# Performance work log

Measured on AMD Instinct MI355X. Metric: run time of the kernel, lower is better.

The kernel has to match this reference:

```python
import jax, jax.numpy as jnp
import numpy as np

N_NODES = 50000
N_EDGES = 800000
H = 128   # atom_hidden_feats
B = 64    # bond_in_feats
NEG_SLOPE = 0.01  # torch LeakyReLU default


def setup_inputs() -> dict:
    key = jax.random.key(0)
    k1, k2, k3, k4, k5 = jax.random.split(key, 5)
    feat = jax.random.normal(k1, (N_NODES, H), dtype=jnp.float32)
    gdf_feat = jax.random.normal(k2, (N_EDGES, B), dtype=jnp.float32)
    # Linear(2H+B -> H): weight [H, 2H+B], bias [H]
    W = jax.random.normal(k3, (H, 2 * H + B), dtype=jnp.float32) * 0.05
    b = jnp.zeros((H,), dtype=jnp.float32)
    src = jax.random.randint(k4, (N_EDGES,), 0, N_NODES, dtype=jnp.int64)
    dst = jax.random.randint(k5, (N_EDGES,), 0, N_NODES, dtype=jnp.int64)
    return {"feat": feat, "gdf_feat": gdf_feat, "W": W, "b": b, "src": src, "dst": dst}


def reference(feat, gdf_feat, W, b, src, dst):
    n_nodes = feat.shape[0]
    # Per-edge message: concat(src_feat, dst_feat, edge_feat) -> linear -> gate
    z = jnp.concatenate([feat[src], feat[dst], gdf_feat], axis=-1)  # [E, 2H+B]
    z = z @ W.T + b                                                 # [E, H]
    msg = jax.nn.sigmoid(z) * jnp.where(z > 0, z, NEG_SLOPE * z)    # sigmoid * leaky_relu
    # Scatter-sum messages to destination nodes
    return jax.ops.segment_sum(msg, dst, num_segments=n_nodes)      # [N, H]
```

## Files before the change

### kernel.cpp

```cpp
#include <hip/hip_runtime.h>
#include <hip/hip_bf16.h>

typedef __attribute__((ext_vector_type(8)))  short bf16x8;
typedef __attribute__((ext_vector_type(16))) float f32x16;
typedef __attribute__((ext_vector_type(4)))  float f32x4;
typedef __attribute__((ext_vector_type(2)))  __fp16 fp16x2;

#define NN 50000
#define EE 800000
#define HH 128
#define KK 320
#define NEG 0.01f
#define NTILES (EE / 64)
#define NBLK 512
#define ACC_BYTES ((size_t)NN * HH * 2)

__device__ __forceinline__ unsigned pack2(float a, float b) {
    unsigned short lo = __builtin_bit_cast(unsigned short, __float2bfloat16(a));
    unsigned short hi = __builtin_bit_cast(unsigned short, __float2bfloat16(b));
    return (unsigned)lo | ((unsigned)hi << 16);
}

__global__ __launch_bounds__(256) void featcvt_kernel(const float* __restrict__ feat,
                                                      ushort* __restrict__ featb)
{
    const int t = blockIdx.x * 256 + threadIdx.x;
    const float* p = feat + (long long)t * 8;
    f32x4 v0 = *(const f32x4*)p;
    f32x4 v1 = *(const f32x4*)(p + 4);
    int4 h;
    h.x = (int)pack2(v0[0], v0[1]); h.y = (int)pack2(v0[2], v0[3]);
    h.z = (int)pack2(v1[0], v1[1]); h.w = (int)pack2(v1[2], v1[3]);
    *(int4*)(featb + (long long)t * 8) = h;
}

__global__ __launch_bounds__(256, 2) void fused_pipe_kernel(
    const ushort* __restrict__ featb, const float* __restrict__ gdf,
    const float*  __restrict__ W,     const float* __restrict__ bias,
    const int*    __restrict__ src,   const int*   __restrict__ dst,
    __fp16* __restrict__ acc16)
{
    __shared__ int4 lds4[2][64 * 40];
    __shared__ int  dsts[2][64];

    const int tid  = threadIdx.x;
    const int lane = tid & 63;
    const int wid  = tid >> 6;
    const int col  = wid * 32 + (lane & 31);
    const int khalf = lane >> 5;
    const int r = tid >> 2, q = tid & 3;

    bf16x8 Wb[20];
    {
        const float* wrow = W + col * KK + khalf * 8;
        #pragma unroll
        for (int k = 0; k < 20; k++) {
            f32x4 x0 = *(const f32x4*)(wrow + k * 16);
            f32x4 x1 = *(const f32x4*)(wrow + k * 16 + 4);
            union { bf16x8 v; unsigned u[4]; } t;
            t.u[0] = pack2(x0[0], x0[1]); t.u[1] = pack2(x0[2], x0[3]);
            t.u[2] = pack2(x1[0], x1[1]); t.u[3] = pack2(x1[2], x1[3]);
            Wb[k] = t.v;
        }
    }
    const float bv = bias[col];

    int4  sf[8];
    f32x4 sg[4];
    int   dStage;

    auto issueLoads = [&](int t, int s_i, int d_i) {
        const ushort* fs = featb + (long long)s_i * HH;
        const ushort* fd = featb + (long long)d_i * HH;
        const float*  ge = gdf + ((long long)t * 64 + r) * 64;
        #pragma unroll
        for (int i = 0; i < 8; i++) {
            const int c = q + i * 4;
            sf[i] = *(const int4*)((c < 16) ? (fs + c * 8) : (fd + (c - 16) * 8));
        }
        #pragma unroll
        for (int i = 0; i < 2; i++) {
            const int cg = q + i * 4;
            sg[2 * i]     = *(const f32x4*)(ge + cg * 8);
            sg[2 * i + 1] = *(const f32x4*)(ge + cg * 8 + 4);
        }
    };
    auto writeStage = [&](int buf) {
        char* base = (char*)lds4[buf];
        const int xr = (r & 7) << 4;
        #pragma unroll
        for (int i = 0; i < 8; i++) {
            const int c = q + i * 4;
            *(int4*)(base + r * 640 + ((c * 16) ^ xr)) = sf[i];
        }
        #pragma unroll
        for (int i = 0; i < 2; i++) {
            const int c = 32 + q + i * 4;
            int4 h;
            h.x = (int)pack2(sg[2*i][0], sg[2*i][1]);
            h.y = (int)pack2(sg[2*i][2], sg[2*i][3]);
            h.z = (int)pack2(sg[2*i+1][0], sg[2*i+1][1]);
            h.w = (int)pack2(sg[2*i+1][2], sg[2*i+1][3]);
            *(int4*)(base + r * 640 + ((c * 16) ^ xr)) = h;
        }
        if (q == 0) dsts[buf][r] = dStage;
    };

    int tile = blockIdx.x;
    int sN = src[(long long)tile * 64 + r];
    int dN = dst[(long long)tile * 64 + r];
    issueLoads(tile, sN, dN);
    dStage = dN;
    int nt = tile + NBLK;
    {
        const int tc = (nt < NTILES) ? nt : 0;
        sN = src[(long long)tc * 64 + r];
        dN = dst[(long long)tc * 64 + r];
    }
    writeStage(0);
    __syncthreads();

    int cur = 0;
    const int arow = lane & 31;
    const int xa   = (arow & 7) << 4;

    while (true) {
        const bool hasNext = (nt < NTILES);
        if (hasNext) {
            issueLoads(nt, sN, dN);
            dStage = dN;
            const int nnt = nt + NBLK;
            const int tc = (nnt < NTILES) ? nnt : 0;
            sN = src[(long long)tc * 64 + r];
            dN = dst[(long long)tc * 64 + r];
        }

        char* abase = (char*)lds4[cur];
        f32x16 acc0 = {}; f32x16 acc1 = {};
        #pragma unroll
        for (int k = 0; k < 20; k++) {
            const int kb = k * 32 + khalf * 16;
            bf16x8 a0 = *(const bf16x8*)(abase + arow * 640 + (kb ^ xa));
            bf16x8 a1 = *(const bf16x8*)(abase + (arow + 32) * 640 + (kb ^ xa));
            acc0 = __builtin_amdgcn_mfma_f32_32x32x16_bf16(a0, Wb[k], acc0, 0, 0, 0);
            acc1 = __builtin_amdgcn_mfma_f32_32x32x16_bf16(a1, Wb[k], acc1, 0, 0, 0);
        }

        #pragma unroll
        for (int rt = 0; rt < 2; rt++) {
            const f32x16 A = rt ? acc1 : acc0;
            #pragma unroll
            for (int g = 0; g < 4; g++) {
                #pragma unroll
                for (int j = 0; j < 4; j++) {
                    const int reg = g * 4 + j;
                    const int row = j + g * 8 + khalf * 4;
                    const float z  = A[reg] + bv;
                    const float lr = z > 0.f ? z : NEG * z;
                    const float sg2 = 1.f / (1.f + __expf(-z));
                    const float m  = lr * sg2;
                    const float o  = __shfl_xor(m, 1);
                    const int dn = dsts[cur][rt * 32 + row];
                    if (!(lane & 1)) {
                        fp16x2 hv = __builtin_amdgcn_cvt_pkrtz(m, o);
                        __fp16* p = acc16 + (long long)dn * HH + col;
                        asm volatile("global_atomic_pk_add_f16 %0, %1, off"
                                     :: "v"(p), "v"(hv) : "memory");
                    }
                }
            }
        }

        if (!hasNext) break;
        writeStage(cur ^ 1);
        tile = nt; nt += NBLK; cur ^= 1;
        __syncthreads();
    }
}

__global__ __launch_bounds__(256) void fused_fallback_kernel(
    const float* __restrict__ feat, const float* __restrict__ gdf,
    const float* __restrict__ W,    const float* __restrict__ bias,
    const int*   __restrict__ src,  const int*   __restrict__ dst,
    float* __restrict__ out)
{
    __shared__ int4 lds4[64 * 40];
    __shared__ int  dsts[64];
    char* lds = (char*)lds4;
    const int tid = threadIdx.x, lane = tid & 63, wid = tid >> 6;
    const int col = wid * 32 + (lane & 31), khalf = lane >> 5;
    const int r = tid >> 2, q = tid & 3;
    const long long ebase = (long long)blockIdx.x * 64;

    bf16x8 Wb[20];
    {
        const float* wrow = W + col * KK + khalf * 8;
        #pragma unroll
        for (int k = 0; k < 20; k++) {
            f32x4 x0 = *(const f32x4*)(wrow + k * 16);
            f32x4 x1 = *(const f32x4*)(wrow + k * 16 + 4);
            union { bf16x8 v; unsigned u[4]; } t;
            t.u[0] = pack2(x0[0], x0[1]); t.u[1] = pack2(x0[2], x0[3]);
            t.u[2] = pack2(x1[0], x1[1]); t.u[3] = pack2(x1[2], x1[3]);
            Wb[k] = t.v;
        }
    }
    const int s = src[ebase + r], d = dst[ebase + r];
    if (q == 0) dsts[r] = d;
    {
        const float* fs = feat + (long long)s * HH;
        const float* fd = feat + (long long)d * HH;
        const float* ge = gdf + (ebase + r) * 64;
        #pragma unroll
        for (int i = 0; i < 10; i++) {
            const int c = q + i * 4;
            const float* p = (c < 16) ? (fs + c * 8)
                           : (c < 32) ? (fd + (c - 16) * 8)
                                      : (ge + (c - 32) * 8);
            f32x4 v0 = *(const f32x4*)p;
            f32x4 v1 = *(const f32x4*)(p + 4);
            int4 h;
            h.x = (int)pack2(v0[0], v0[1]); h.y = (int)pack2(v0[2], v0[3]);
            h.z = (int)pack2(v1[0], v1[1]); h.w = (int)pack2(v1[2], v1[3]);
            *(int4*)(lds + r * 640 + ((c * 16) ^ ((r & 7) << 4))) = h;
        }
    }
    __syncthreads();
    f32x16 acc0 = {}; f32x16 acc1 = {};
    const int arow = lane & 31, xa = (arow & 7) << 4;
    #pragma unroll
    for (int k = 0; k < 20; k++) {
        const int kb = k * 32 + khalf * 16;
        bf16x8 a0 = *(const bf16x8*)(lds + arow * 640 + (kb ^ xa));
        bf16x8 a1 = *(const bf16x8*)(lds + (arow + 32) * 640 + (kb ^ xa));
        acc0 = __builtin_amdgcn_mfma_f32_32x32x16_bf16(a0, Wb[k], acc0, 0, 0, 0);
        acc1 = __builtin_amdgcn_mfma_f32_32x32x16_bf16(a1, Wb[k], acc1, 0, 0, 0);
    }
    const float bv = bias[col];
    #pragma unroll
    for (int rt = 0; rt < 2; rt++) {
        const f32x16 A = rt ? acc1 : acc0;
        #pragma unroll
        for (int g = 0; g < 4; g++) {
            #pragma unroll
            for (int j = 0; j < 4; j++) {
                const int reg = g * 4 + j;
                const int row = j + g * 8 + khalf * 4;
                const float z  = A[reg] + bv;
                const float lr = z > 0.f ? z : NEG * z;
                const float sgm = 1.f / (1.f + __expf(-z));
                unsafeAtomicAdd(out + (long long)dsts[rt * 32 + row] * HH + col, lr * sgm);
            }
        }
    }
}

__global__ __launch_bounds__(256) void conv_kernel(const int4* __restrict__ acc,
                                                   float4* __restrict__ out)
{
    const int i = blockIdx.x * 256 + threadIdx.x;
    union { int4 v; __fp16 h[8]; } u;
    u.v = acc[i];
    float4 a, b;
    a.x = (float)u.h[0]; a.y = (float)u.h[1]; a.z = (float)u.h[2]; a.w = (float)u.h[3];
    b.x = (float)u.h[4]; b.y = (float)u.h[5]; b.z = (float)u.h[6]; b.w = (float)u.h[7];
    out[2 * i]     = a;
    out[2 * i + 1] = b;
}

extern "C" void kernel_launch(void* const* d_in, const int* in_sizes, int n_in,
                              void* d_out, int out_size, void* d_ws, size_t ws_size,
                              hipStream_t stream) {
    const float* feat = (const float*)d_in[0];
    const float* gdf  = (const float*)d_in[1];
    const float* W    = (const float*)d_in[2];
    const float* bias = (const float*)d_in[3];
    const int*   src  = (const int*)d_in[4];
    const int*   dst  = (const int*)d_in[5];
    float* out = (float*)d_out;

    __fp16* acc16 = (__fp16*)d_ws;
    ushort* featb = (ushort*)((char*)d_ws + ACC_BYTES);

    if (ws_size >= 2 * ACC_BYTES) {
        (void)hipMemsetAsync(d_ws, 0, ACC_BYTES, stream);
        featcvt_kernel<<<NN * HH / 8 / 256, 256, 0, stream>>>(feat, featb);
        fused_pipe_kernel<<<NBLK, 256, 0, stream>>>(featb, gdf, W, bias,
                                                    src, dst, acc16);
        conv_kernel<<<NN * HH / 8 / 256, 256, 0, stream>>>((const int4*)d_ws,
                                                           (float4*)out);
    } else {
        (void)hipMemsetAsync(out, 0, (size_t)out_size * sizeof(float), stream);
        fused_fallback_kernel<<<EE / 64, 256, 0, stream>>>(feat, gdf, W, bias,
                                                           src, dst, out);
    }
}
```

Before: 355.4 us.

## Single-buffer LDS stage to fit three blocks per CU with explicit barriers

Replaces the double-buffered LDS tile with a single buffer and guards it with explicit s_barrier plus lgkmcnt waits, which lets launch bounds rise to 3 blocks per CU and the persistent grid grow to 768 blocks. It also loads the four destination indices as one int4 and swaps the inline-asm packed fp16 atomic for unsafeAtomicAdd on __half2 with round-to-nearest conversion. The aim is more latency hiding for the gathers and atomics. In exchange it adds an extra barrier per tile, and the register cap that comes with 3 waves/SIMD may cause spills of the 20 W fragments.

```diff
diff --git a/kernel.cpp b/kernel.cpp
--- a/kernel.cpp
+++ b/kernel.cpp
@@ -1,10 +1,10 @@
 #include <hip/hip_runtime.h>
 #include <hip/hip_bf16.h>
+#include <hip/hip_fp16.h>
 
 typedef __attribute__((ext_vector_type(8)))  short bf16x8;
 typedef __attribute__((ext_vector_type(16))) float f32x16;
 typedef __attribute__((ext_vector_type(4)))  float f32x4;
-typedef __attribute__((ext_vector_type(2)))  __fp16 fp16x2;
 
 #define NN 50000
 #define EE 800000
@@ -12,7 +12,7 @@
 #define KK 320
 #define NEG 0.01f
 #define NTILES (EE / 64)
-#define NBLK 512
+#define NBLK 768
 #define ACC_BYTES ((size_t)NN * HH * 2)
 
 __device__ __forceinline__ unsigned pack2(float a, float b) {
@@ -34,14 +34,14 @@
     *(int4*)(featb + (long long)t * 8) = h;
 }
 
-__global__ __launch_bounds__(256, 2) void fused_pipe_kernel(
+__global__ __launch_bounds__(256, 3) void fused_pipe_kernel(
     const ushort* __restrict__ featb, const float* __restrict__ gdf,
     const float*  __restrict__ W,     const float* __restrict__ bias,
     const int*    __restrict__ src,   const int*   __restrict__ dst,
     __fp16* __restrict__ acc16)
 {
-    __shared__ int4 lds4[2][64 * 40];
-    __shared__ int  dsts[2][64];
+    __shared__ char lds[64 * 640 + 256];
+    int* dsts = (int*)(lds + 64 * 640);
 
     const int tid  = threadIdx.x;
     const int lane = tid & 63;
@@ -66,13 +66,13 @@
     const float bv = bias[col];
 
     int4  sf[8];
-    f32x4 sg[4];
+    f32x4 sgv[4];
     int   dStage;
 
-    auto issueLoads = [&](int t, int s_i, int d_i) {
+    auto issueLoads = [&](long long t, int s_i, int d_i) {
         const ushort* fs = featb + (long long)s_i * HH;
         const ushort* fd = featb + (long long)d_i * HH;
-        const float*  ge = gdf + ((long long)t * 64 + r) * 64;
+        const float*  ge = gdf + (t * 64 + r) * 64;
         #pragma unroll
         for (int i = 0; i < 8; i++) {
             const int c = q + i * 4;
@@ -81,46 +81,48 @@
         #pragma unroll
         for (int i = 0; i < 2; i++) {
             const int cg = q + i * 4;
-            sg[2 * i]     = *(const f32x4*)(ge + cg * 8);
-            sg[2 * i + 1] = *(const f32x4*)(ge + cg * 8 + 4);
+            sgv[2 * i]     = *(const f32x4*)(ge + cg * 8);
+            sgv[2 * i + 1] = *(const f32x4*)(ge + cg * 8 + 4);
         }
     };
-    auto writeStage = [&](int buf) {
-        char* base = (char*)lds4[buf];
+    auto writeStage = [&]() {
         const int xr = (r & 7) << 4;
         #pragma unroll
         for (int i = 0; i < 8; i++) {
             const int c = q + i * 4;
-            *(int4*)(base + r * 640 + ((c * 16) ^ xr)) = sf[i];
+            *(int4*)(lds + r * 640 + ((c * 16) ^ xr)) = sf[i];
         }
         #pragma unroll
         for (int i = 0; i < 2; i++) {
             const int c = 32 + q + i * 4;
             int4 h;
-            h.x = (int)pack2(sg[2*i][0], sg[2*i][1]);
-            h.y = (int)pack2(sg[2*i][2], sg[2*i][3]);
-            h.z = (int)pack2(sg[2*i+1][0], sg[2*i+1][1]);
-            h.w = (int)pack2(sg[2*i+1][2], sg[2*i+1][3]);
-            *(int4*)(base + r * 640 + ((c * 16) ^ xr)) = h;
-        }
-        if (q == 0) dsts[buf][r] = dStage;
+            h.x = (int)pack2(sgv[2*i][0], sgv[2*i][1]);
+            h.y = (int)pack2(sgv[2*i][2], sgv[2*i][3]);
+            h.z = (int)pack2(sgv[2*i+1][0], sgv[2*i+1][1]);
+            h.w = (int)pack2(sgv[2*i+1][2], sgv[2*i+1][3]);
+            *(int4*)(lds + r * 640 + ((c * 16) ^ xr)) = h;
+        }
+        if (q == 0) dsts[r] = dStage;
     };
 
     int tile = blockIdx.x;
-    int sN = src[(long long)tile * 64 + r];
-    int dN = dst[(long long)tile * 64 + r];
-    issueLoads(tile, sN, dN);
-    dStage = dN;
+    {
+        int s0 = src[(long long)tile * 64 + r];
+        int d0 = dst[(long long)tile * 64 + r];
+        issueLoads(tile, s0, d0);
+        dStage = d0;
+    }
     int nt = tile + NBLK;
-    {
-        const int tc = (nt < NTILES) ? nt : 0;
-        sN = src[(long long)tc * 64 + r];
-        dN = dst[(long long)tc * 64 + r];
-    }
-    writeStage(0);
-    __syncthreads();
-
-    int cur = 0;
+    int sN, dN;
+    {
+        const long long tc = (nt < NTILES) ? nt : 0;
+        sN = src[tc * 64 + r]; dN = dst[tc * 64 + r];
+    }
+    writeStage();
+    asm volatile("s_waitcnt lgkmcnt(0)" ::: "memory");
+    __builtin_amdgcn_sched_barrier(0);
+    __builtin_amdgcn_s_barrier();
+
     const int arow = lane & 31;
     const int xa   = (arow & 7) << 4;
 
@@ -129,19 +131,16 @@
         if (hasNext) {
             issueLoads(nt, sN, dN);
             dStage = dN;
-            const int nnt = nt + NBLK;
-            const int tc = (nnt < NTILES) ? nnt : 0;
-            sN = src[(long long)tc * 64 + r];
-            dN = dst[(long long)tc * 64 + r];
-        }
-
-        char* abase = (char*)lds4[cur];
+            const long long tc = (nt + NBLK < NTILES) ? (long long)(nt + NBLK) : 0;
+            sN = src[tc * 64 + r]; dN = dst[tc * 64 + r];
+        }
+
         f32x16 acc0 = {}; f32x16 acc1 = {};
         #pragma unroll
         for (int k = 0; k < 20; k++) {
             const int kb = k * 32 + khalf * 16;
-            bf16x8 a0 = *(const bf16x8*)(abase + arow * 640 + (kb ^ xa));
-            bf16x8 a1 = *(const bf16x8*)(abase + (arow + 32) * 640 + (kb ^ xa));
+            bf16x8 a0 = *(const bf16x8*)(lds + arow * 640 + (kb ^ xa));
+            bf16x8 a1 = *(const bf16x8*)(lds + (arow + 32) * 640 + (kb ^ xa));
             acc0 = __builtin_amdgcn_mfma_f32_32x32x16_bf16(a0, Wb[k], acc0, 0, 0, 0);
             acc1 = __builtin_amdgcn_mfma_f32_32x32x16_bf16(a1, Wb[k], acc1, 0, 0, 0);
         }
@@ -151,30 +150,32 @@
             const f32x16 A = rt ? acc1 : acc0;
             #pragma unroll
             for (int g = 0; g < 4; g++) {
+                const int4 dn4 = *(const int4*)(dsts + rt * 32 + g * 8 + khalf * 4);
                 #pragma unroll
                 for (int j = 0; j < 4; j++) {
                     const int reg = g * 4 + j;
-                    const int row = j + g * 8 + khalf * 4;
                     const float z  = A[reg] + bv;
                     const float lr = z > 0.f ? z : NEG * z;
-                    const float sg2 = 1.f / (1.f + __expf(-z));
-                    const float m  = lr * sg2;
+                    const float sgm = 1.f / (1.f + __expf(-z));
+                    const float m  = lr * sgm;
                     const float o  = __shfl_xor(m, 1);
-                    const int dn = dsts[cur][rt * 32 + row];
+                    const int dn = ((const int*)&dn4)[j];
                     if (!(lane & 1)) {
-                        fp16x2 hv = __builtin_amdgcn_cvt_pkrtz(m, o);
-                        __fp16* p = acc16 + (long long)dn * HH + col;
-                        asm volatile("global_atomic_pk_add_f16 %0, %1, off"
-                                     :: "v"(p), "v"(hv) : "memory");
+                        __half2 hv = __float22half2_rn(float2{m, o});
+                        unsafeAtomicAdd((__half2*)(acc16 + (long long)dn * HH + col), hv);
                     }
                 }
             }
         }
 
         if (!hasNext) break;
-        writeStage(cur ^ 1);
-        tile = nt; nt += NBLK; cur ^= 1;
-        __syncthreads();
+        __builtin_amdgcn_s_barrier();
+        __builtin_amdgcn_sched_barrier(0);
+        writeStage();
+        asm volatile("s_waitcnt lgkmcnt(0)" ::: "memory");
+        __builtin_amdgcn_sched_barrier(0);
+        __builtin_amdgcn_s_barrier();
+        tile = nt; nt += NBLK;
     }
 }
 
```

Result: slower. 382.9 us (+7.7%).
